# Kernel optimization log

Hardware: AMD Instinct MI355X
Metric: run time of the kernel (lower is better)

The kernel has to match this reference:

```python
import jax, jax.numpy as jnp
import numpy as np

N_NODES = 50000
N_EDGES = 1000000
N_GRAPHS = 256
ORIG = 92
ATOM = 64
NBR = 41
EPS = 1e-5


def _bn_train(h, gamma, beta):
    # BatchNorm1d in training mode: batch stats, biased variance
    mu = h.mean(axis=0)
    var = jnp.var(h, axis=0)
    return (h - mu) * jax.lax.rsqrt(var + EPS) * gamma + beta


def setup_inputs() -> dict:
    key = jax.random.key(0)
    ks = jax.random.split(key, 16)
    inp = {
        "x": jax.random.normal(ks[0], (N_NODES, ORIG), dtype=jnp.float32),
        "edge_attr": jax.random.normal(ks[1], (N_EDGES, NBR), dtype=jnp.float32),
        "lower_f": jax.random.normal(ks[2], (N_NODES, ATOM), dtype=jnp.float32),
        "edge_index": jax.random.randint(ks[3], (2, N_EDGES), 0, N_NODES, dtype=jnp.int32),
        "batch": jnp.sort(jax.random.randint(ks[4], (N_NODES,), 0, N_GRAPHS, dtype=jnp.int32)),
        # params
        "emb_W": jax.random.normal(ks[5], (ORIG, ATOM), dtype=jnp.float32) / np.sqrt(ORIG),
        "emb_b": jnp.zeros((ATOM,), dtype=jnp.float32),
        "fc_W": jax.random.normal(ks[6], (2 * ATOM + NBR, 2 * ATOM), dtype=jnp.float32) / np.sqrt(2 * ATOM + NBR),
        "fc_b": jnp.zeros((2 * ATOM,), dtype=jnp.float32),
        "bn1_g": jnp.ones((2 * ATOM,), dtype=jnp.float32),
        "bn1_b": jnp.zeros((2 * ATOM,), dtype=jnp.float32),
        "bn2_g": jnp.ones((ATOM,), dtype=jnp.float32),
        "bn2_b": jnp.zeros((ATOM,), dtype=jnp.float32),
        "att_W": jax.random.normal(ks[7], (ATOM, 1), dtype=jnp.float32) / np.sqrt(ATOM),
        "att_b": jnp.zeros((1,), dtype=jnp.float32),
        "out_W": jax.random.normal(ks[8], (ATOM, 1), dtype=jnp.float32) / np.sqrt(ATOM),
        "out_b": jnp.zeros((1,), dtype=jnp.float32),
    }
    return inp


def reference(x, edge_attr, lower_f, emb_W, emb_b, fc_W, fc_b, bn1_g, bn1_b,
              bn2_g, bn2_b, att_W, att_b, out_W, out_b, edge_index, batch):
    # embedding + lower-level features
    atom_fea = x @ emb_W + emb_b + lower_f  # [N, ATOM]

    # CGConv: gather endpoints, concat with edge features
    src, dst = edge_index[0], edge_index[1]
    total = jnp.concatenate([atom_fea[src], atom_fea[dst], edge_attr], axis=-1)  # [E, 2A+NBR]
    gated = _bn_train(total @ fc_W + fc_b, bn1_g, bn1_b)  # [E, 2A]
    nbr_filter, nbr_core = gated[:, :ATOM], gated[:, ATOM:]
    msg = jax.nn.sigmoid(nbr_filter) * jax.nn.softplus(nbr_core)  # [E, A]
    summed = jax.ops.segment_sum(msg, src, num_segments=N_NODES)  # [N, A]
    atom_out = _bn_train(summed, bn2_g, bn2_b)

    # SiLU + attentional aggregation per graph
    h = jax.nn.silu(atom_out)  # [N, A]
    logits = (h @ att_W + att_b)[:, 0]  # [N]
    seg_max = jax.ops.segment_max(logits, batch, num_segments=N_GRAPHS)
    e = jnp.exp(logits - seg_max[batch])
    denom = jax.ops.segment_sum(e, batch, num_segments=N_GRAPHS)
    alpha = e / denom[batch]  # [N]
    crys = jax.ops.segment_sum(alpha[:, None] * h, batch, num_segments=N_GRAPHS)  # [G, A]
    crys_fea = crys @ out_W + out_b  # [G, 1]
    return atom_out, crys_fea
```

## Files before the change

kernel.cpp:

```cpp
#include <hip/hip_runtime.h>
#include <math.h>

#define NN 50000
#define NE 1000000
#define NG 256
#define ORIGD 92
#define NBRD 41
#define NSPREAD 32
#define SCAN_B 256

typedef unsigned short u16;
typedef __attribute__((ext_vector_type(8))) short short8;
typedef __attribute__((ext_vector_type(4))) float f32x4;

#define OFF_AFB     0
#define OFF_SUMMED  1600000
#define OFF_WT      4800000
#define OFF_BN1SPR  4812288
#define OFF_BN1SC   4820480
#define OFF_BN2ACC  4820736
#define OFF_BN2SC   4820864
#define OFF_ELOG    4820992
#define OFF_SEGMAX  4870992
#define OFF_DENOM   4871248
#define OFF_CNT     4871504
#define OFF_PTR     4921504
#define OFF_HEAD    4971504
#define OFF_BSUM    5021504
#define OFF_BOFS    5021760
#define OFF_EIDX    5022016
#define OFF_H       6022016
#define OFF_T2_END  70022016

__device__ __forceinline__ u16 f2b(float f) {
    unsigned u = __float_as_uint(f);
    return (u16)((u + 0x7FFFu + ((u >> 16) & 1u)) >> 16);
}
__device__ __forceinline__ float b2f(u16 u) {
    return __uint_as_float(((unsigned)u) << 16);
}
__device__ __forceinline__ float gate(float f, float cc) {
    float sig = __builtin_amdgcn_rcpf(1.f + __expf(-f));
    float sp  = fmaxf(cc, 0.f) + __logf(1.f + __expf(-fabsf(cc)));
    return sig * sp;
}
__device__ __forceinline__ float fsilu(float x) {
    return x * __builtin_amdgcn_rcpf(1.f + __expf(-x));
}

__global__ __launch_bounds__(256) void k_embed(
    const float* __restrict__ x, const float* __restrict__ lf,
    const float* __restrict__ W, const float* __restrict__ b,
    u16* __restrict__ afb)
{
    int gid = blockIdx.x * 256 + threadIdx.x;
    int n = gid >> 6, c = gid & 63;
    const float* xr = x + (long)n * ORIGD;
    float acc = b[c] + lf[gid];
#pragma unroll 4
    for (int k = 0; k < ORIGD; k++)
        acc = fmaf(xr[k], W[k * 64 + c], acc);
    afb[gid] = f2b(acc);
}

__global__ void k_prepw(const float* __restrict__ fcW, u16* __restrict__ wT)
{
    int i = blockIdx.x * 256 + threadIdx.x;
    int j = i / 192, k = i - j * 192;
    wT[i] = (k < 169) ? f2b(fcW[k * 128 + j]) : (u16)0;
}

__global__ void k_hist(const int* __restrict__ ei, int* __restrict__ cnt)
{
    int e = blockIdx.x * 256 + threadIdx.x;
    if (e < NE) atomicAdd(&cnt[ei[e]], 1);
}

__global__ void k_partial(const int* __restrict__ cnt, int* __restrict__ lofs,
                          int* __restrict__ bsum)
{
    __shared__ int sd[SCAN_B];
    int t = threadIdx.x, b = blockIdx.x, n = b * SCAN_B + t;
    int v = (n < NN) ? cnt[n] : 0;
    sd[t] = v; __syncthreads();
    for (int o = 1; o < SCAN_B; o <<= 1) {
        int x = (t >= o) ? sd[t - o] : 0;
        __syncthreads();
        sd[t] += x;
        __syncthreads();
    }
    if (n < NN) lofs[n] = sd[t] - v;
    if (t == SCAN_B - 1) bsum[b] = sd[t];
}

__global__ void k_scanb(const int* __restrict__ bsum, int* __restrict__ bofs, int nb)
{
    __shared__ int sd[256];
    int t = threadIdx.x;
    int v = (t < nb) ? bsum[t] : 0;
    sd[t] = v; __syncthreads();
    for (int o = 1; o < 256; o <<= 1) {
        int x = (t >= o) ? sd[t - o] : 0;
        __syncthreads();
        sd[t] += x;
        __syncthreads();
    }
    bofs[t] = sd[t] - v;
}

__global__ void k_addofs(int* __restrict__ ptr, const int* __restrict__ bofs,
                         int* __restrict__ head)
{
    int n = blockIdx.x * 256 + threadIdx.x;
    if (n < NN) {
        int p = ptr[n] + bofs[n >> 8];
        ptr[n] = p; head[n] = p;
    }
}

__global__ void k_fill(const int* __restrict__ ei, int* __restrict__ head,
                       int* __restrict__ eidx)
{
    int e = blockIdx.x * 256 + threadIdx.x;
    if (e < NE) {
        int pos = atomicAdd(&head[ei[e]], 1);
        eidx[pos] = e;
    }
}

__global__ __launch_bounds__(256) void k_gemm_h(
    const u16* __restrict__ afb, const float* __restrict__ ea,
    const int* __restrict__ ei, const u16* __restrict__ wT,
    u16* __restrict__ h, float* __restrict__ spread)
{
    __shared__ __align__(16) u16 sTl[64 * 200];
    __shared__ int sSrc[64], sDst[64];
    const int tid = threadIdx.x;
    const int e0 = blockIdx.x * 64;

    if (tid < 64) sSrc[tid] = ei[e0 + tid];
    else if (tid < 128) sDst[tid - 64] = ei[NE + e0 + tid - 64];
    __syncthreads();

    for (int i = tid; i < 1024; i += 256) {
        int e = i >> 4, q = i & 15;
        const u16* g = (q < 8) ? (afb + (long)sSrc[e] * 64 + q * 8)
                               : (afb + (long)sDst[e] * 64 + (q - 8) * 8);
        *(short8*)(sTl + e * 200 + q * 8) = *(const short8*)g;
    }
    for (int i = tid; i < 64 * 64; i += 256) {
        int e = i >> 6, c = i & 63;
        float v = (c < NBRD) ? ea[(long)(e0 + e) * NBRD + c] : 0.f;
        sTl[e * 200 + 128 + c] = f2b(v);
    }
    __syncthreads();

    const int lane = tid & 63, w = tid >> 6;
    const int n16 = lane & 15, quad = lane >> 4;

    short8 A0[6], A1[6];
    {
        const u16* b0 = wT + (16 * w + n16) * 192 + quad * 8;
        const u16* b1 = wT + (16 * (w + 4) + n16) * 192 + quad * 8;
#pragma unroll
        for (int ks = 0; ks < 6; ks++) {
            A0[ks] = *(const short8*)(b0 + ks * 32);
            A1[ks] = *(const short8*)(b1 + ks * 32);
        }
    }

    const int j0 = 16 * w + 4 * quad;
    float s0[4] = {0,0,0,0}, q0[4] = {0,0,0,0}, s1[4] = {0,0,0,0}, q1[4] = {0,0,0,0};

    for (int t = 0; t < 4; t++) {
        const u16* row = sTl + (16 * t + n16) * 200 + quad * 8;
        f32x4 acc0 = {0.f, 0.f, 0.f, 0.f}, acc1 = {0.f, 0.f, 0.f, 0.f};
#pragma unroll
        for (int ks = 0; ks < 6; ks++) {
            short8 b = *(const short8*)(row + ks * 32);
            acc0 = __builtin_amdgcn_mfma_f32_16x16x32_bf16(A0[ks], b, acc0, 0, 0, 0);
            acc1 = __builtin_amdgcn_mfma_f32_16x16x32_bf16(A1[ks], b, acc1, 0, 0, 0);
        }
#pragma unroll
        for (int r = 0; r < 4; r++) {
            s0[r] += acc0[r]; q0[r] = fmaf(acc0[r], acc0[r], q0[r]);
            s1[r] += acc1[r]; q1[r] = fmaf(acc1[r], acc1[r], q1[r]);
        }
        int ge = e0 + 16 * t + n16;
        u16* hp = h + (long)ge * 128 + j0;
        ushort4 v0 = make_ushort4(f2b(acc0[0]), f2b(acc0[1]), f2b(acc0[2]), f2b(acc0[3]));
        ushort4 v1 = make_ushort4(f2b(acc1[0]), f2b(acc1[1]), f2b(acc1[2]), f2b(acc1[3]));
        *(ushort4*)hp = v0;
        *(ushort4*)(hp + 64) = v1;
    }

#pragma unroll
    for (int m = 1; m < 16; m <<= 1) {
#pragma unroll
        for (int r = 0; r < 4; r++) {
            s0[r] += __shfl_xor(s0[r], m); q0[r] += __shfl_xor(q0[r], m);
            s1[r] += __shfl_xor(s1[r], m); q1[r] += __shfl_xor(q1[r], m);
        }
    }
    if (n16 == 0) {
        float* sp = spread + (blockIdx.x & (NSPREAD - 1)) * 256;
#pragma unroll
        for (int r = 0; r < 4; r++) {
            atomicAdd(sp + j0 + r,       s0[r]);
            atomicAdd(sp + 128 + j0 + r, q0[r]);
            atomicAdd(sp + 64 + j0 + r,  s1[r]);
            atomicAdd(sp + 192 + j0 + r, q1[r]);
        }
    }
}

template <int MODE>
__global__ __launch_bounds__(256) void k_gemm(
    const u16* __restrict__ afb, const float* __restrict__ ea,
    const int* __restrict__ ei, const u16* __restrict__ wT,
    const float* __restrict__ sc, float* __restrict__ outbuf)
{
    __shared__ __align__(16) u16 sTl[64 * 200];
    __shared__ int sSrc[64], sDst[64];
    const int tid = threadIdx.x;
    const int e0 = blockIdx.x * 64;

    if (tid < 64) sSrc[tid] = ei[e0 + tid];
    else if (tid < 128) sDst[tid - 64] = ei[NE + e0 + tid - 64];
    __syncthreads();
    for (int i = tid; i < 1024; i += 256) {
        int e = i >> 4, q = i & 15;
        const u16* g = (q < 8) ? (afb + (long)sSrc[e] * 64 + q * 8)
                               : (afb + (long)sDst[e] * 64 + (q - 8) * 8);
        *(short8*)(sTl + e * 200 + q * 8) = *(const short8*)g;
    }
    for (int i = tid; i < 64 * 64; i += 256) {
        int e = i >> 6, c = i & 63;
        float v = (c < NBRD) ? ea[(long)(e0 + e) * NBRD + c] : 0.f;
        sTl[e * 200 + 128 + c] = f2b(v);
    }
    __syncthreads();

    const int lane = tid & 63, w = tid >> 6;
    const int n16 = lane & 15, quad = lane >> 4;
    short8 A0[6], A1[6];
    {
        const u16* b0 = wT + (16 * w + n16) * 192 + quad * 8;
        const u16* b1 = wT + (16 * (w + 4) + n16) * 192 + quad * 8;
#pragma unroll
        for (int ks = 0; ks < 6; ks++) {
            A0[ks] = *(const short8*)(b0 + ks * 32);
            A1[ks] = *(const short8*)(b1 + ks * 32);
        }
    }
    const int j0 = 16 * w + 4 * quad;
    float s0[4] = {0,0,0,0}, q0[4] = {0,0,0,0}, s1[4] = {0,0,0,0}, q1[4] = {0,0,0,0};
    float scf[4], shf[4], scc[4], shc[4];
    if (MODE == 1) {
#pragma unroll
        for (int r = 0; r < 4; r++) {
            scf[r] = sc[j0 + r];        shf[r] = sc[128 + j0 + r];
            scc[r] = sc[64 + j0 + r];   shc[r] = sc[192 + j0 + r];
        }
    }
    for (int t = 0; t < 4; t++) {
        const u16* row = sTl + (16 * t + n16) * 200 + quad * 8;
        f32x4 acc0 = {0.f, 0.f, 0.f, 0.f}, acc1 = {0.f, 0.f, 0.f, 0.f};
#pragma unroll
        for (int ks = 0; ks < 6; ks++) {
            short8 b = *(const short8*)(row + ks * 32);
            acc0 = __builtin_amdgcn_mfma_f32_16x16x32_bf16(A0[ks], b, acc0, 0, 0, 0);
            acc1 = __builtin_amdgcn_mfma_f32_16x16x32_bf16(A1[ks], b, acc1, 0, 0, 0);
        }
        if (MODE == 0) {
#pragma unroll
            for (int r = 0; r < 4; r++) {
                s0[r] += acc0[r]; q0[r] = fmaf(acc0[r], acc0[r], q0[r]);
                s1[r] += acc1[r]; q1[r] = fmaf(acc1[r], acc1[r], q1[r]);
            }
        } else {
            int src = sSrc[16 * t + n16];
            float* dst = outbuf + (long)src * 64 + j0;
#pragma unroll
            for (int r = 0; r < 4; r++) {
                float f  = fmaf(acc0[r], scf[r], shf[r]);
                float cc = fmaf(acc1[r], scc[r], shc[r]);
                atomicAdd(dst + r, gate(f, cc));
            }
        }
    }
    if (MODE == 0) {
#pragma unroll
        for (int m = 1; m < 16; m <<= 1) {
#pragma unroll
            for (int r = 0; r < 4; r++) {
                s0[r] += __shfl_xor(s0[r], m); q0[r] += __shfl_xor(q0[r], m);
                s1[r] += __shfl_xor(s1[r], m); q1[r] += __shfl_xor(q1[r], m);
            }
        }
        if (n16 == 0) {
            float* sp = outbuf + (blockIdx.x & (NSPREAD - 1)) * 256;
#pragma unroll
            for (int r = 0; r < 4; r++) {
                atomicAdd(sp + j0 + r,       s0[r]);
                atomicAdd(sp + 128 + j0 + r, q0[r]);
                atomicAdd(sp + 64 + j0 + r,  s1[r]);
                atomicAdd(sp + 192 + j0 + r, q1[r]);
            }
        }
    }
}

__global__ void k_bn1fin(const float* __restrict__ spread,
                         const float* __restrict__ g, const float* __restrict__ b,
                         float* __restrict__ sc)
{
    int c = threadIdx.x;
    float s = 0.f, q = 0.f;
    for (int k = 0; k < NSPREAD; k++) { s += spread[k * 256 + c]; q += spread[k * 256 + 128 + c]; }
    float mean_acc = s / (float)NE;
    float var = q / (float)NE - mean_acc * mean_acc;
    float scale = g[c] * rsqrtf(var + 1e-5f);
    sc[c] = scale;
    sc[128 + c] = b[c] - mean_acc * scale;
}

__global__ __launch_bounds__(256) void k_scatter(
    const u16* __restrict__ h, const int* __restrict__ ptr,
    const int* __restrict__ cnt, const int* __restrict__ eidx,
    const float* __restrict__ sc, float* __restrict__ summed)
{
    int tid = threadIdx.x;
    int n = blockIdx.x * 4 + (tid >> 6);
    int l = tid & 63;
    int es = l & 7, cg = l >> 3;

    float4 a0 = *(const float4*)(sc + cg * 8);
    float4 a1 = *(const float4*)(sc + cg * 8 + 4);
    float4 b0 = *(const float4*)(sc + 128 + cg * 8);
    float4 b1 = *(const float4*)(sc + 128 + cg * 8 + 4);
    float4 c0 = *(const float4*)(sc + 64 + cg * 8);
    float4 c1 = *(const float4*)(sc + 64 + cg * 8 + 4);
    float4 d0 = *(const float4*)(sc + 192 + cg * 8);
    float4 d1 = *(const float4*)(sc + 192 + cg * 8 + 4);
    float scf[8] = {a0.x,a0.y,a0.z,a0.w,a1.x,a1.y,a1.z,a1.w};
    float shf[8] = {b0.x,b0.y,b0.z,b0.w,b1.x,b1.y,b1.z,b1.w};
    float scc[8] = {c0.x,c0.y,c0.z,c0.w,c1.x,c1.y,c1.z,c1.w};
    float shc[8] = {d0.x,d0.y,d0.z,d0.w,d1.x,d1.y,d1.z,d1.w};

    int p0 = ptr[n], deg = cnt[n];
    float acc[8] = {0,0,0,0,0,0,0,0};
    for (int i = 0; i < deg; i += 8) {
        int idx = i + es;
        bool valid = idx < deg;
        int e = eidx[p0 + (valid ? idx : 0)];
        const u16* hr = h + (long)e * 128;
        short8 f8 = *(const short8*)(hr + cg * 8);
        short8 c8 = *(const short8*)(hr + 64 + cg * 8);
#pragma unroll
        for (int j = 0; j < 8; j++) {
            float f  = fmaf(b2f((u16)f8[j]), scf[j], shf[j]);
            float cc = fmaf(b2f((u16)c8[j]), scc[j], shc[j]);
            float g  = gate(f, cc);
            acc[j] += valid ? g : 0.f;
        }
    }
#pragma unroll
    for (int m = 1; m < 8; m <<= 1)
#pragma unroll
        for (int j = 0; j < 8; j++) acc[j] += __shfl_xor(acc[j], m);
    if (es == 0) {
        float* sp = summed + (long)n * 64 + cg * 8;
        float4 v0 = {acc[0], acc[1], acc[2], acc[3]};
        float4 v1 = {acc[4], acc[5], acc[6], acc[7]};
        *(float4*)sp = v0;
        *(float4*)(sp + 4) = v1;
    }
}

__global__ __launch_bounds__(256) void k_bn2stats(const float* __restrict__ summed,
                                                  float* __restrict__ acc2)
{
    int tid = threadIdx.x; int c = tid & 63; int sub = tid >> 6;
    float s = 0.f, q = 0.f;
    for (int r = blockIdx.x * 4 + sub; r < NN; r += 4 * 128) {
        float v = summed[(long)r * 64 + c]; s += v; q = fmaf(v, v, q);
    }
    __shared__ float rs[256], rq[256];
    rs[tid] = s; rq[tid] = q; __syncthreads();
    if (tid < 64) {
        s = rs[tid] + rs[tid + 64] + rs[tid + 128] + rs[tid + 192];
        q = rq[tid] + rq[tid + 64] + rq[tid + 128] + rq[tid + 192];
        atomicAdd(&acc2[tid], s);
        atomicAdd(&acc2[64 + tid], q);
    }
}

__global__ void k_bn2fin(const float* __restrict__ acc2,
                         const float* __restrict__ g, const float* __restrict__ b,
                         float* __restrict__ sc2, const float* __restrict__ outb,
                         float* __restrict__ out)
{
    int c = threadIdx.x;
    if (c < 64) {
        float mean = acc2[c] / (float)NN;
        float var = acc2[64 + c] / (float)NN - mean * mean;
        float scale = g[c] * rsqrtf(var + 1e-5f);
        sc2[c] = scale;
        sc2[64 + c] = b[c] - mean * scale;
    }
    out[(long)NN * 64 + c] = outb[0];
}

__global__ __launch_bounds__(256) void k_nodepost(
    const float* __restrict__ summed, const float* __restrict__ sc2,
    const float* __restrict__ attW, const float* __restrict__ attb,
    const int* __restrict__ batch, float* __restrict__ out,
    float* __restrict__ elog, unsigned* __restrict__ segmax)
{
    int tid = threadIdx.x; int n = blockIdx.x * 4 + (tid >> 6); int c = tid & 63;
    float v = summed[(long)n * 64 + c];
    float ao = fmaf(v, sc2[c], sc2[64 + c]);
    out[(long)n * 64 + c] = ao;
    float h = fsilu(ao);
    float p = h * attW[c];
#pragma unroll
    for (int off = 32; off; off >>= 1) p += __shfl_down(p, off, 64);
    if (c == 0) {
        float logit = p + attb[0];
        elog[n] = logit;
        unsigned u = __float_as_uint(logit);
        u = (u & 0x80000000u) ? ~u : (u | 0x80000000u);
        atomicMax(&segmax[batch[n]], u);
    }
}

__global__ void k_denom(const int* __restrict__ batch,
                        const unsigned* __restrict__ segmax,
                        float* __restrict__ elog, float* __restrict__ denom)
{
    int n = blockIdx.x * 256 + threadIdx.x;
    if (n >= NN) return;
    int b = batch[n];
    unsigned u = segmax[b];
    u = (u & 0x80000000u) ? (u & 0x7FFFFFFFu) : ~u;
    float e = __expf(elog[n] - __uint_as_float(u));
    elog[n] = e;
    atomicAdd(&denom[b], e);
}

__global__ __launch_bounds__(256) void k_crys(
    const float* __restrict__ atom_out, const float* __restrict__ elog,
    const float* __restrict__ denom, const int* __restrict__ batch,
    const float* __restrict__ outW, float* __restrict__ out)
{
    int tid = threadIdx.x; int n = blockIdx.x * 4 + (tid >> 6); int l = tid & 63;
    int b = batch[n];
    float alpha = elog[n] / denom[b];
    float ao = atom_out[(long)n * 64 + l];
    float p = fsilu(ao) * outW[l];
#pragma unroll
    for (int off = 32; off; off >>= 1) p += __shfl_down(p, off, 64);
    if (l == 0) atomicAdd(&out[(long)NN * 64 + b], alpha * p);
}

extern "C" void kernel_launch(void* const* d_in, const int* in_sizes, int n_in,
                              void* d_out, int out_size, void* d_ws, size_t ws_size,
                              hipStream_t stream)
{
    const float* x    = (const float*)d_in[0];
    const float* eatt = (const float*)d_in[1];
    const float* lf   = (const float*)d_in[2];
    const int*   ei   = (const int*)d_in[3];
    const int*   batch= (const int*)d_in[4];
    const float* embW = (const float*)d_in[5];
    const float* embB = (const float*)d_in[6];
    const float* fcW  = (const float*)d_in[7];
    const float* bn1g = (const float*)d_in[9];
    const float* bn1b = (const float*)d_in[10];
    const float* bn2g = (const float*)d_in[11];
    const float* bn2b = (const float*)d_in[12];
    const float* attW = (const float*)d_in[13];
    const float* attB = (const float*)d_in[14];
    const float* outW = (const float*)d_in[15];
    const float* outB = (const float*)d_in[16];
    float* out = (float*)d_out;
    float* ws  = (float*)d_ws;

    u16* afb  = (u16*)(ws + OFF_AFB);
    u16* wT   = (u16*)(ws + OFF_WT);
    int* cnt  = (int*)(ws + OFF_CNT);
    int* ptr  = (int*)(ws + OFF_PTR);
    int* head = (int*)(ws + OFF_HEAD);
    int* bsum = (int*)(ws + OFF_BSUM);
    int* bofs = (int*)(ws + OFF_BOFS);
    int* eidx = (int*)(ws + OFF_EIDX);
    u16* h    = (u16*)(ws + OFF_H);

    const bool t2 = ws_size >= (size_t)OFF_T2_END * sizeof(float);

    k_embed<<<12500, 256, 0, stream>>>(x, lf, embW, embB, afb);
    k_prepw<<<96, 256, 0, stream>>>(fcW, wT);

    if (t2) {
        hipMemsetAsync(ws + OFF_BN1SPR, 0,
                       (size_t)(OFF_PTR - OFF_BN1SPR) * sizeof(float), stream);
        k_hist<<<(NE + 255) / 256, 256, 0, stream>>>(ei, cnt);
        k_partial<<<(NN + SCAN_B - 1) / SCAN_B, SCAN_B, 0, stream>>>(cnt, ptr, bsum);
        k_scanb<<<1, 256, 0, stream>>>(bsum, bofs, (NN + SCAN_B - 1) / SCAN_B);
        k_addofs<<<(NN + 255) / 256, 256, 0, stream>>>(ptr, bofs, head);
        k_fill<<<(NE + 255) / 256, 256, 0, stream>>>(ei, head, eidx);
        k_gemm_h<<<NE / 64, 256, 0, stream>>>(afb, eatt, ei, wT, h, ws + OFF_BN1SPR);
        k_bn1fin<<<1, 128, 0, stream>>>(ws + OFF_BN1SPR, bn1g, bn1b, ws + OFF_BN1SC);
        k_scatter<<<NN / 4, 256, 0, stream>>>(h, ptr, cnt, eidx, ws + OFF_BN1SC,
                                              ws + OFF_SUMMED);
    } else {
        hipMemsetAsync(ws + OFF_SUMMED, 0,
                       (size_t)(OFF_PTR - OFF_SUMMED) * sizeof(float), stream);
        k_gemm<0><<<NE / 64, 256, 0, stream>>>(afb, eatt, ei, wT, ws + OFF_BN1SC,
                                               ws + OFF_BN1SPR);
        k_bn1fin<<<1, 128, 0, stream>>>(ws + OFF_BN1SPR, bn1g, bn1b, ws + OFF_BN1SC);
        k_gemm<1><<<NE / 64, 256, 0, stream>>>(afb, eatt, ei, wT, ws + OFF_BN1SC,
                                               ws + OFF_SUMMED);
    }

    k_bn2stats<<<128, 256, 0, stream>>>(ws + OFF_SUMMED, ws + OFF_BN2ACC);
    k_bn2fin<<<1, 256, 0, stream>>>(ws + OFF_BN2ACC, bn2g, bn2b, ws + OFF_BN2SC,
                                    outB, out);
    k_nodepost<<<12500, 256, 0, stream>>>(ws + OFF_SUMMED, ws + OFF_BN2SC, attW, attB,
                                          batch, out, ws + OFF_ELOG,
                                          (unsigned*)(ws + OFF_SEGMAX));
    k_denom<<<196, 256, 0, stream>>>(batch, (const unsigned*)(ws + OFF_SEGMAX),
                                     ws + OFF_ELOG, ws + OFF_DENOM);
    k_crys<<<12500, 256, 0, stream>>>(out, ws + OFF_ELOG, ws + OFF_DENOM, batch,
                                      outW, out);
}
```

Baseline: 1.218 ms.

## Precompute per-node projections of atom features before edge GEMM

```diff
diff --git a/kernel.cpp b/kernel.cpp
--- a/kernel.cpp
+++ b/kernel.cpp
@@ -31,6 +31,8 @@
 #define OFF_EIDX    5022016
 #define OFF_H       6022016
 #define OFF_T2_END  70022016
+#define OFF_P       70022016
+#define OFF_T3_END  82822016
 
 __device__ __forceinline__ u16 f2b(float f) {
     unsigned u = __float_as_uint(f);
@@ -68,6 +70,64 @@
     int i = blockIdx.x * 256 + threadIdx.x;
     int j = i / 192, k = i - j * 192;
     wT[i] = (k < 169) ? f2b(fcW[k * 128 + j]) : (u16)0;
+}
+
+__global__ void k_prepw2(const float* __restrict__ fcW, u16* __restrict__ wT3,
+                         u16* __restrict__ wP)
+{
+    int i = blockIdx.x * 256 + threadIdx.x;
+    if (i < 8192) {
+        int j = i >> 6, k = i & 63;
+        wT3[i] = (k < NBRD) ? f2b(fcW[(128 + k) * 128 + j]) : (u16)0;
+    } else {
+        int i2 = i - 8192;
+        int j = i2 >> 6, k = i2 & 63;
+        int row = (j < 128) ? k : (64 + k);
+        wP[i2] = f2b(fcW[row * 128 + (j & 127)]);
+    }
+}
+
+__global__ __launch_bounds__(256) void k_pnode(
+    const u16* __restrict__ afb, const u16* __restrict__ wP, float* __restrict__ P)
+{
+    __shared__ __align__(16) u16 sB[64 * 72];
+    const int tid = threadIdx.x;
+    const int n0 = blockIdx.x * 64;
+
+    for (int i = tid; i < 512; i += 256) {
+        int r = i >> 3, c = i & 7;
+        int n = n0 + r;
+        short8 v = {0,0,0,0,0,0,0,0};
+        if (n < NN) v = *(const short8*)(afb + (long)n * 64 + c * 8);
+        *(short8*)(sB + r * 72 + c * 8) = v;
+    }
+    __syncthreads();
+
+    const int lane = tid & 63, w = tid >> 6;
+    const int n16 = lane & 15, quad = lane >> 4;
+    short8 A[4][2];
+#pragma unroll
+    for (int m = 0; m < 4; m++) {
+        const u16* base = wP + (16 * (w + 4 * m) + n16) * 64 + quad * 8;
+        A[m][0] = *(const short8*)(base);
+        A[m][1] = *(const short8*)(base + 32);
+    }
+    for (int t = 0; t < 4; t++) {
+        const u16* row = sB + (16 * t + n16) * 72 + quad * 8;
+        short8 b0 = *(const short8*)(row);
+        short8 b1 = *(const short8*)(row + 32);
+        int n = n0 + 16 * t + n16;
+#pragma unroll
+        for (int m = 0; m < 4; m++) {
+            f32x4 acc = {0.f, 0.f, 0.f, 0.f};
+            acc = __builtin_amdgcn_mfma_f32_16x16x32_bf16(A[m][0], b0, acc, 0, 0, 0);
+            acc = __builtin_amdgcn_mfma_f32_16x16x32_bf16(A[m][1], b1, acc, 0, 0, 0);
+            if (n < NN) {
+                int j = 16 * (w + 4 * m) + 4 * quad;
+                *(f32x4*)(P + (long)n * 256 + j) = acc;
+            }
+        }
+    }
 }
 
 __global__ void k_hist(const int* __restrict__ ei, int* __restrict__ cnt)
@@ -125,6 +185,96 @@
     if (e < NE) {
         int pos = atomicAdd(&head[ei[e]], 1);
         eidx[pos] = e;
+    }
+}
+
+__global__ __launch_bounds__(256) void k_gemm_h2(
+    const float* __restrict__ ea, const int* __restrict__ ei,
+    const u16* __restrict__ wT3, const float* __restrict__ P,
+    u16* __restrict__ h, float* __restrict__ spread)
+{
+    __shared__ __align__(16) u16 sTl[64 * 72];
+    __shared__ int sSrc[64], sDst[64];
+    const int tid = threadIdx.x;
+    const int e0 = blockIdx.x * 64;
+
+    if (tid < 64) sSrc[tid] = ei[e0 + tid];
+    else if (tid < 128) sDst[tid - 64] = ei[NE + e0 + tid - 64];
+
+    for (int i = tid; i < 64 * 64; i += 256) {
+        int e = i >> 6, c = i & 63;
+        float v = (c < NBRD) ? ea[(long)(e0 + e) * NBRD + c] : 0.f;
+        sTl[e * 72 + c] = f2b(v);
+    }
+    __syncthreads();
+
+    const int lane = tid & 63, w = tid >> 6;
+    const int n16 = lane & 15, quad = lane >> 4;
+
+    short8 A0[2], A1[2];
+    {
+        const u16* b0 = wT3 + (16 * w + n16) * 64 + quad * 8;
+        const u16* b1 = wT3 + (16 * (w + 4) + n16) * 64 + quad * 8;
+        A0[0] = *(const short8*)(b0);  A0[1] = *(const short8*)(b0 + 32);
+        A1[0] = *(const short8*)(b1);  A1[1] = *(const short8*)(b1 + 32);
+    }
+
+    const int j0 = 16 * w + 4 * quad;
+    float s0[4] = {0,0,0,0}, q0[4] = {0,0,0,0}, s1[4] = {0,0,0,0}, q1[4] = {0,0,0,0};
+
+    for (int t = 0; t < 4; t++) {
+        const int ge16 = 16 * t + n16;
+        const int src = sSrc[ge16], dst = sDst[ge16];
+        const float* pS = P + (long)src * 256;
+        const float* pD = P + (long)dst * 256 + 128;
+        f32x4 g0 = *(const f32x4*)(pS + j0);
+        f32x4 g1 = *(const f32x4*)(pS + 64 + j0);
+        f32x4 g2 = *(const f32x4*)(pD + j0);
+        f32x4 g3 = *(const f32x4*)(pD + 64 + j0);
+
+        const u16* row = sTl + ge16 * 72 + quad * 8;
+        short8 b0 = *(const short8*)(row);
+        short8 b1 = *(const short8*)(row + 32);
+        f32x4 acc0 = {0.f, 0.f, 0.f, 0.f}, acc1 = {0.f, 0.f, 0.f, 0.f};
+        acc0 = __builtin_amdgcn_mfma_f32_16x16x32_bf16(A0[0], b0, acc0, 0, 0, 0);
+        acc0 = __builtin_amdgcn_mfma_f32_16x16x32_bf16(A0[1], b1, acc0, 0, 0, 0);
+        acc1 = __builtin_amdgcn_mfma_f32_16x16x32_bf16(A1[0], b0, acc1, 0, 0, 0);
+        acc1 = __builtin_amdgcn_mfma_f32_16x16x32_bf16(A1[1], b1, acc1, 0, 0, 0);
+
+        u16 hv0[4], hv1[4];
+#pragma unroll
+        for (int r = 0; r < 4; r++) {
+            float u0 = acc0[r] + g0[r] + g2[r];
+            float u1 = acc1[r] + g1[r] + g3[r];
+            s0[r] += u0; q0[r] = fmaf(u0, u0, q0[r]);
+            s1[r] += u1; q1[r] = fmaf(u1, u1, q1[r]);
+            hv0[r] = f2b(u0); hv1[r] = f2b(u1);
+        }
+        int ge = e0 + ge16;
+        u16* hp = h + (long)ge * 128 + j0;
+        ushort4 v0 = make_ushort4(hv0[0], hv0[1], hv0[2], hv0[3]);
+        ushort4 v1 = make_ushort4(hv1[0], hv1[1], hv1[2], hv1[3]);
+        *(ushort4*)hp = v0;
+        *(ushort4*)(hp + 64) = v1;
+    }
+
+#pragma unroll
+    for (int m = 1; m < 16; m <<= 1) {
+#pragma unroll
+        for (int r = 0; r < 4; r++) {
+            s0[r] += __shfl_xor(s0[r], m); q0[r] += __shfl_xor(q0[r], m);
+            s1[r] += __shfl_xor(s1[r], m); q1[r] += __shfl_xor(q1[r], m);
+        }
+    }
+    if (n16 == 0) {
+        float* sp = spread + (blockIdx.x & (NSPREAD - 1)) * 256;
+#pragma unroll
+        for (int r = 0; r < 4; r++) {
+            atomicAdd(sp + j0 + r,       s0[r]);
+            atomicAdd(sp + 128 + j0 + r, q0[r]);
+            atomicAdd(sp + 64 + j0 + r,  s1[r]);
+            atomicAdd(sp + 192 + j0 + r, q1[r]);
+        }
     }
 }
 
@@ -497,12 +647,30 @@
     int* eidx = (int*)(ws + OFF_EIDX);
     u16* h    = (u16*)(ws + OFF_H);
 
+    const bool t3 = ws_size >= (size_t)OFF_T3_END * sizeof(float);
     const bool t2 = ws_size >= (size_t)OFF_T2_END * sizeof(float);
 
     k_embed<<<12500, 256, 0, stream>>>(x, lf, embW, embB, afb);
-    k_prepw<<<96, 256, 0, stream>>>(fcW, wT);
-
-    if (t2) {
+
+    if (t3) {
+        u16* wT3 = wT;
+        u16* wP  = wT + 8192;
+        float* P = ws + OFF_P;
+        k_prepw2<<<96, 256, 0, stream>>>(fcW, wT3, wP);
+        hipMemsetAsync(ws + OFF_BN1SPR, 0,
+                       (size_t)(OFF_PTR - OFF_BN1SPR) * sizeof(float), stream);
+        k_hist<<<(NE + 255) / 256, 256, 0, stream>>>(ei, cnt);
+        k_partial<<<(NN + SCAN_B - 1) / SCAN_B, SCAN_B, 0, stream>>>(cnt, ptr, bsum);
+        k_scanb<<<1, 256, 0, stream>>>(bsum, bofs, (NN + SCAN_B - 1) / SCAN_B);
+        k_addofs<<<(NN + 255) / 256, 256, 0, stream>>>(ptr, bofs, head);
+        k_fill<<<(NE + 255) / 256, 256, 0, stream>>>(ei, head, eidx);
+        k_pnode<<<(NN + 63) / 64, 256, 0, stream>>>(afb, wP, P);
+        k_gemm_h2<<<NE / 64, 256, 0, stream>>>(eatt, ei, wT3, P, h, ws + OFF_BN1SPR);
+        k_bn1fin<<<1, 128, 0, stream>>>(ws + OFF_BN1SPR, bn1g, bn1b, ws + OFF_BN1SC);
+        k_scatter<<<NN / 4, 256, 0, stream>>>(h, ptr, cnt, eidx, ws + OFF_BN1SC,
+                                              ws + OFF_SUMMED);
+    } else if (t2) {
+        k_prepw<<<96, 256, 0, stream>>>(fcW, wT);
         hipMemsetAsync(ws + OFF_BN1SPR, 0,
                        (size_t)(OFF_PTR - OFF_BN1SPR) * sizeof(float), stream);
         k_hist<<<(NE + 255) / 256, 256, 0, stream>>>(ei, cnt);
@@ -515,6 +683,7 @@
         k_scatter<<<NN / 4, 256, 0, stream>>>(h, ptr, cnt, eidx, ws + OFF_BN1SC,
                                               ws + OFF_SUMMED);
     } else {
+        k_prepw<<<96, 256, 0, stream>>>(fcW, wT);
         hipMemsetAsync(ws + OFF_SUMMED, 0,
                        (size_t)(OFF_PTR - OFF_SUMMED) * sizeof(float), stream);
         k_gemm<0><<<NE / 64, 256, 0, stream>>>(afb, eatt, ei, wT, ws + OFF_BN1SC,
```

Result: no change. 1.241 ms (+1.9%).
